# Kernel optimization log

Measured on AMD Instinct MI355X. Metric: run time of the kernel, lower is better.

## Reference

```python
import jax, jax.numpy as jnp
import numpy as np

EMBED_DIM = 768
NUM_HEADS = 12
HEAD_DIM = EMBED_DIM // NUM_HEADS
SCALING = HEAD_DIM ** -0.5
B, N = 4, 2048


def setup_inputs() -> dict:
    key = jax.random.key(0)
    k_x, k_wqkv, k_bqkv, k_wo, k_bo = jax.random.split(key, 5)
    s = EMBED_DIM ** -0.5
    return {
        "x_q": jax.random.normal(k_x, (B, N, EMBED_DIM), dtype=jnp.float32),
        # torch Linear weight layout: (out_features, in_features)
        "w_qkv": jax.random.normal(k_wqkv, (3 * EMBED_DIM, EMBED_DIM), dtype=jnp.float32) * s,
        "b_qkv": jax.random.normal(k_bqkv, (3 * EMBED_DIM,), dtype=jnp.float32) * s,
        "w_out": jax.random.normal(k_wo, (EMBED_DIM, EMBED_DIM), dtype=jnp.float32) * s,
        "b_out": jax.random.normal(k_bo, (EMBED_DIM,), dtype=jnp.float32) * s,
    }


def reference(x_q, w_qkv, b_qkv, w_out, b_out):
    b_sz, n, _ = x_q.shape
    # qkv projection: x @ W^T + b -> (B, N, 3E)
    qkv = jnp.einsum("bne,fe->bnf", x_q, w_qkv) + b_qkv
    # reshape to (B, N, 3, H, D) then move heads: (B, H, 3, N, D)
    qkv = qkv.reshape(b_sz, n, 3, NUM_HEADS, HEAD_DIM).transpose(0, 3, 2, 1, 4)
    q, k, v = qkv[:, :, 0], qkv[:, :, 1], qkv[:, :, 2]
    q = q * SCALING
    # scores (B, H, N, N); att_m == 'Aug' adds constant +1 bias
    attn = jnp.einsum("bhqd,bhkd->bhqk", q, k) + 1.0
    attn = jax.nn.softmax(attn, axis=-1)
    # attn_dropout p=0.0 -> identity
    out = jnp.einsum("bhqk,bhkd->bhqd", attn, v)
    out = out.transpose(0, 2, 1, 3).reshape(b_sz, n, EMBED_DIM)
    return jnp.einsum("bne,fe->bnf", out, w_out) + b_out
```

## Files before the change

kernel.cpp:

```cpp
#include <hip/hip_runtime.h>

typedef unsigned short u16;
typedef unsigned int   u32;
typedef __bf16 bf16x4 __attribute__((ext_vector_type(4)));
typedef __bf16 bf16x8 __attribute__((ext_vector_type(8)));
typedef float  f32x4  __attribute__((ext_vector_type(4)));

__device__ __forceinline__ u16 f2bf(float f) {
  u32 u = __float_as_uint(f);
  u32 r = (u + 0x7fffu + ((u >> 16) & 1u)) >> 16;
  return (u16)r;
}

__device__ __forceinline__ float fexp2(float x) {
  return __builtin_amdgcn_exp2f(x);
}

typedef const __attribute__((address_space(1))) u32* gp1;
typedef __attribute__((address_space(3))) u32* lp3;
__device__ __forceinline__ void gload16(const void* g, void* l) {
  __builtin_amdgcn_global_load_lds((gp1)g, (lp3)l, 16, 0, 0);
}

__device__ __forceinline__ f32x4 mfma16(bf16x8 a, bf16x8 b, f32x4 c) {
  return __builtin_amdgcn_mfma_f32_16x16x32_bf16(a, b, c, 0, 0, 0);
}

__device__ __forceinline__ int swz8(int r) { return (r ^ (r >> 3)) & 7; }

__global__ __launch_bounds__(256) void cast_all(const float* __restrict__ x,
                                                const float* __restrict__ wqkv,
                                                const float* __restrict__ wo,
                                                uint4* __restrict__ dst) {
  int i = blockIdx.x * 256 + threadIdx.x;
  if (i >= 1081344) return;
  const float* s;
  int j;
  if (i < 786432)       { s = x;    j = i; }
  else if (i < 1007616) { s = wqkv; j = i - 786432; }
  else                  { s = wo;   j = i - 1007616; }
  const float4* s4 = (const float4*)s;
  float4 a = s4[2 * j], b = s4[2 * j + 1];
  uint4 o;
  o.x = (u32)f2bf(a.x) | ((u32)f2bf(a.y) << 16);
  o.y = (u32)f2bf(a.z) | ((u32)f2bf(a.w) << 16);
  o.z = (u32)f2bf(b.x) | ((u32)f2bf(b.y) << 16);
  o.w = (u32)f2bf(b.z) | ((u32)f2bf(b.w) << 16);
  dst[i] = o;
}

__global__ __launch_bounds__(256) void gemm_qkv(
    const u16* __restrict__ A, const u16* __restrict__ Bm,
    const float* __restrict__ bias,
    u16* __restrict__ Q, u16* __restrict__ K, u16* __restrict__ V) {
  __shared__ u16 As[128 * 64];
  __shared__ u16 Bs[128 * 64];
  const int tid = threadIdx.x, w = tid >> 6, l = tid & 63;
  const int lr = l & 15, lg = l >> 4;
  const int n0 = blockIdx.x * 128, m0 = blockIdx.y * 128;
  const int wr = (w >> 1) * 64, wc = (w & 1) * 64;
  f32x4 acc[4][4] = {};
  for (int kt = 0; kt < 768; kt += 64) {
    __syncthreads();
    const u16* Ab = A + m0 * 768 + kt;
    const u16* Bb = Bm + n0 * 768 + kt;
#pragma unroll
    for (int i = 0; i < 4; ++i) {
      int c = i * 256 + tid;
      int r = c >> 3, q = c & 7;
      int qs = (q ^ swz8(r)) << 3;
      gload16(Ab + r * 768 + qs, (char*)As + c * 16);
      gload16(Bb + r * 768 + qs, (char*)Bs + c * 16);
    }
    __syncthreads();
    bf16x8 af[4][2], bfr[4][2];
#pragma unroll
    for (int m = 0; m < 4; ++m) {
      int row = wr + m * 16 + lr;
      int sw = swz8(row);
#pragma unroll
      for (int ks = 0; ks < 2; ++ks)
        af[m][ks] = *(const bf16x8*)((char*)As + row * 128 +
                                     (((ks * 4 + lg) ^ sw) << 4));
    }
#pragma unroll
    for (int n = 0; n < 4; ++n) {
      int row = wc + n * 16 + lr;
      int sw = swz8(row);
#pragma unroll
      for (int ks = 0; ks < 2; ++ks)
        bfr[n][ks] = *(const bf16x8*)((char*)Bs + row * 128 +
                                      (((ks * 4 + lg) ^ sw) << 4));
    }
#pragma unroll
    for (int ks = 0; ks < 2; ++ks)
#pragma unroll
      for (int m = 0; m < 4; ++m)
#pragma unroll
        for (int n = 0; n < 4; ++n)
          acc[m][n] = mfma16(af[m][ks], bfr[n][ks], acc[m][n]);
  }
#pragma unroll
  for (int n = 0; n < 4; ++n) {
    int f = n0 + wc + n * 16 + lr;
    float bv = bias[f];
    int three = f / 768;
    int hd = f - three * 768;
    int h = hd >> 6, dd = hd & 63;
    if (three == 2) {
#pragma unroll
      for (int m = 0; m < 4; ++m) {
        int row0 = m0 + wr + m * 16 + lg * 4;
        int b2 = row0 >> 11, ns = row0 & 2047;
        ushort4 pk;
        pk.x = f2bf(acc[m][n][0] + bv);
        pk.y = f2bf(acc[m][n][1] + bv);
        pk.z = f2bf(acc[m][n][2] + bv);
        pk.w = f2bf(acc[m][n][3] + bv);
        *(ushort4*)&V[((size_t)(b2 * 12 + h) * 64 + dd) * 2048 + ns] = pk;
      }
    } else {
      u16* dst = (three == 0) ? Q : K;
      float sc = (three == 0) ? 0.125f * 1.44269504f : 1.0f;
#pragma unroll
      for (int m = 0; m < 4; ++m) {
        int row0 = m0 + wr + m * 16 + lg * 4;
#pragma unroll
        for (int j = 0; j < 4; ++j) {
          int row = row0 + j;
          int b2 = row >> 11, ns = row & 2047;
          float val = (acc[m][n][j] + bv) * sc;
          dst[(((b2 * 12 + h) * 2048 + ns) << 6) + dd] = f2bf(val);
        }
      }
    }
  }
}

__global__ __launch_bounds__(256, 4) void attn_kernel(
    const u16* __restrict__ Q, const u16* __restrict__ K,
    const u16* __restrict__ Vt, u16* __restrict__ O) {
  __shared__ u16 Ks[2][64 * 64];
  __shared__ u16 Vs[2][64 * 64];
  const int tid = threadIdx.x, w = tid >> 6, l = tid & 63;
  const int lr = l & 15, lg = l >> 4;
  int d0i = blockIdx.x;
  int bi = (d0i & 7) * 96 + (d0i >> 3);
  int qt = bi & 15, h = (bi >> 4) % 12, b = bi / 192;
  const u16* Qp = Q + ((size_t)(b * 12 + h) * 2048 + qt * 128) * 64;
  const u16* Kp = K + (size_t)(b * 12 + h) * 2048 * 64;
  const u16* Vp = Vt + (size_t)(b * 12 + h) * 64 * 2048;
  u16* Op = O + (size_t)(b * 2048 + qt * 128) * 768 + h * 64;

  bf16x8 aq[2][2];
#pragma unroll
  for (int mt = 0; mt < 2; ++mt)
#pragma unroll
    for (int ks = 0; ks < 2; ++ks)
      aq[mt][ks] = *(const bf16x8*)&Qp[(w * 32 + mt * 16 + lr) * 64 + ks * 32 + lg * 8];

  bf16x8 vone;
#pragma unroll
  for (int i = 0; i < 8; ++i) vone[i] = (__bf16)1.0f;

  f32x4 aO[2][4] = {};
  f32x4 sacc[2] = {};

#define STAGE(buf, kt)                                                         \
  do {                                                                         \
    const u16* Kt = Kp + (kt) * 4096;                                          \
    const u16* Vg = Vp + (kt) * 64;                                            \
    _Pragma("unroll") for (int i = 0; i < 2; ++i) {                            \
      int c = i * 256 + tid;                                                   \
      int r = c >> 3, q = c & 7;                                               \
      int qs = (q ^ swz8(r)) << 3;                                             \
      gload16(Kt + r * 64 + qs, (char*)Ks[buf] + c * 16);                      \
      gload16(Vg + r * 2048 + qs, (char*)Vs[buf] + c * 16);                    \
    }                                                                          \
  } while (0)

  STAGE(0, 0);
  __syncthreads();

#pragma unroll 2
  for (int kt = 0; kt < 32; ++kt) {
    const int p = kt & 1;
    if (kt < 31) STAGE(p ^ 1, kt + 1);

    f32x4 S[2][4] = {};
    __builtin_amdgcn_s_setprio(1);
#pragma unroll
    for (int nt = 0; nt < 4; ++nt) {
      int row = nt * 16 + lr;
      int sw = swz8(row);
#pragma unroll
      for (int ks = 0; ks < 2; ++ks) {
        bf16x8 a = *(const bf16x8*)((char*)Ks[p] + row * 128 +
                                    (((ks * 4 + lg) ^ sw) << 4));
        S[0][nt] = mfma16(a, aq[0][ks], S[0][nt]);
        S[1][nt] = mfma16(a, aq[1][ks], S[1][nt]);
      }
    }
    __builtin_amdgcn_s_setprio(0);

    bf16x8 ap[2][2];
#pragma unroll
    for (int mt = 0; mt < 2; ++mt) {
      f32x4 pe[4];
#pragma unroll
      for (int nt = 0; nt < 4; ++nt)
#pragma unroll
        for (int j = 0; j < 4; ++j) pe[nt][j] = fexp2(S[mt][nt][j]);
#pragma unroll
      for (int ks = 0; ks < 2; ++ks) {
        bf16x8 f;
#pragma unroll
        for (int j = 0; j < 4; ++j) {
          f[j]     = (__bf16)pe[2 * ks][j];
          f[4 + j] = (__bf16)pe[2 * ks + 1][j];
        }
        ap[mt][ks] = f;
      }
    }

    __builtin_amdgcn_s_setprio(1);
#pragma unroll
    for (int ks = 0; ks < 2; ++ks) {
      sacc[0] = mfma16(ap[0][ks], vone, sacc[0]);
      sacc[1] = mfma16(ap[1][ks], vone, sacc[1]);
#pragma unroll
      for (int dt = 0; dt < 4; ++dt) {
        int row = dt * 16 + lr;
        int sw = swz8(row);
        char* vrow = (char*)Vs[p] + row * 128 + (lg & 1) * 8;
        bf16x4 lo = *(const bf16x4*)(vrow + (((ks * 4 + (lg >> 1)) ^ sw) << 4));
        bf16x4 hi = *(const bf16x4*)(vrow + (((ks * 4 + 2 + (lg >> 1)) ^ sw) << 4));
        bf16x8 bv = __builtin_shufflevector(lo, hi, 0, 1, 2, 3, 4, 5, 6, 7);
        aO[0][dt] = mfma16(ap[0][ks], bv, aO[0][dt]);
        aO[1][dt] = mfma16(ap[1][ks], bv, aO[1][dt]);
      }
    }
    __builtin_amdgcn_s_setprio(0);

    __syncthreads();
  }

#pragma unroll
  for (int mt = 0; mt < 2; ++mt) {
    f32x4 rinv;
#pragma unroll
    for (int j = 0; j < 4; ++j) rinv[j] = 1.0f / sacc[mt][j];
#pragma unroll
    for (int dt = 0; dt < 4; ++dt)
#pragma unroll
      for (int j = 0; j < 4; ++j) {
        int row = w * 32 + mt * 16 + lg * 4 + j;
        Op[(size_t)row * 768 + dt * 16 + lr] = f2bf(aO[mt][dt][j] * rinv[j]);
      }
  }
}

__global__ __launch_bounds__(256) void gemm_out(
    const u16* __restrict__ A, const u16* __restrict__ Bm,
    const float* __restrict__ bias, float* __restrict__ C) {
  __shared__ u16 As[128 * 64];
  __shared__ u16 Bs[128 * 64];
  const int tid = threadIdx.x, w = tid >> 6, l = tid & 63;
  const int lr = l & 15, lg = l >> 4;
  const int n0 = blockIdx.x * 128, m0 = blockIdx.y * 128;
  const int wr = (w >> 1) * 64, wc = (w & 1) * 64;
  f32x4 acc[4][4] = {};
  for (int kt = 0; kt < 768; kt += 64) {
    __syncthreads();
    const u16* Ab = A + m0 * 768 + kt;
    const u16* Bb = Bm + n0 * 768 + kt;
#pragma unroll
    for (int i = 0; i < 4; ++i) {
      int c = i * 256 + tid;
      int r = c >> 3, q = c & 7;
      int qs = (q ^ swz8(r)) << 3;
      gload16(Ab + r * 768 + qs, (char*)As + c * 16);
      gload16(Bb + r * 768 + qs, (char*)Bs + c * 16);
    }
    __syncthreads();
    bf16x8 af[4][2], bfr[4][2];
#pragma unroll
    for (int m = 0; m < 4; ++m) {
      int row = wr + m * 16 + lr;
      int sw = swz8(row);
#pragma unroll
      for (int ks = 0; ks < 2; ++ks)
        af[m][ks] = *(const bf16x8*)((char*)As + row * 128 +
                                     (((ks * 4 + lg) ^ sw) << 4));
    }
#pragma unroll
    for (int n = 0; n < 4; ++n) {
      int row = wc + n * 16 + lr;
      int sw = swz8(row);
#pragma unroll
      for (int ks = 0; ks < 2; ++ks)
        bfr[n][ks] = *(const bf16x8*)((char*)Bs + row * 128 +
                                      (((ks * 4 + lg) ^ sw) << 4));
    }
#pragma unroll
    for (int ks = 0; ks < 2; ++ks)
#pragma unroll
      for (int m = 0; m < 4; ++m)
#pragma unroll
        for (int n = 0; n < 4; ++n)
          acc[m][n] = mfma16(af[m][ks], bfr[n][ks], acc[m][n]);
  }
#pragma unroll
  for (int n = 0; n < 4; ++n) {
    int f = n0 + wc + n * 16 + lr;
    float bv = bias[f];
#pragma unroll
    for (int m = 0; m < 4; ++m) {
      int row0 = m0 + wr + m * 16 + lg * 4;
#pragma unroll
      for (int j = 0; j < 4; ++j) {
        int row = row0 + j;
        C[(size_t)row * 768 + f] = acc[m][n][j] + bv;
      }
    }
  }
}

extern "C" void kernel_launch(void* const* d_in, const int* in_sizes, int n_in,
                              void* d_out, int out_size, void* d_ws, size_t ws_size,
                              hipStream_t stream) {
  const float* x     = (const float*)d_in[0];
  const float* w_qkv = (const float*)d_in[1];
  const float* b_qkv = (const float*)d_in[2];
  const float* w_out = (const float*)d_in[3];
  const float* b_out = (const float*)d_in[4];

  char* ws = (char*)d_ws;
  u16* xb    = (u16*)(ws + 0);
  u16* wqkvb = (u16*)(ws + 12582912);
  u16* wob   = (u16*)(ws + 16121856);
  u16* qb    = (u16*)(ws + 17301504);
  u16* kb    = (u16*)(ws + 29884416);
  u16* vb    = (u16*)(ws + 42467328);
  u16* ob    = (u16*)(ws + 55050240);

  cast_all<<<4224, 256, 0, stream>>>(x, w_qkv, w_out, (uint4*)ws);

  gemm_qkv<<<dim3(18, 64), 256, 0, stream>>>(xb, wqkvb, b_qkv, qb, kb, vb);
  attn_kernel<<<768, 256, 0, stream>>>(qb, kb, vb, ob);
  gemm_out<<<dim3(6, 64), 256, 0, stream>>>(ob, wob, b_out, (float*)d_out);
}
```

Before: 160.7 us.

## Double-buffer GEMM LDS tiles, remap blocks across XCDs, raise MFMA priority

Both projection GEMMs now use two LDS buffers, so the global-to-LDS load of the next K tile is issued while MFMAs run on the current one. The per-iteration sync count drops from two to one. Blocks are launched on a 1D grid and remapped so consecutive ids spread across the 8 XCDs while neighbouring tiles share cache. s_setprio is raised around the MFMA block. LDS use per block doubles to 64KB, which may lower occupancy.

```diff
diff --git a/kernel.cpp b/kernel.cpp
--- a/kernel.cpp
+++ b/kernel.cpp
@@ -53,26 +53,35 @@
     const u16* __restrict__ A, const u16* __restrict__ Bm,
     const float* __restrict__ bias,
     u16* __restrict__ Q, u16* __restrict__ K, u16* __restrict__ V) {
-  __shared__ u16 As[128 * 64];
-  __shared__ u16 Bs[128 * 64];
+  __shared__ u16 As[2][128 * 64];
+  __shared__ u16 Bs[2][128 * 64];
   const int tid = threadIdx.x, w = tid >> 6, l = tid & 63;
   const int lr = l & 15, lg = l >> 4;
-  const int n0 = blockIdx.x * 128, m0 = blockIdx.y * 128;
+  int id = blockIdx.x;
+  int bi = (id & 7) * 144 + (id >> 3);
+  const int m0 = (bi / 18) * 128, n0 = (bi % 18) * 128;
   const int wr = (w >> 1) * 64, wc = (w & 1) * 64;
   f32x4 acc[4][4] = {};
-  for (int kt = 0; kt < 768; kt += 64) {
-    __syncthreads();
-    const u16* Ab = A + m0 * 768 + kt;
-    const u16* Bb = Bm + n0 * 768 + kt;
-#pragma unroll
-    for (int i = 0; i < 4; ++i) {
-      int c = i * 256 + tid;
-      int r = c >> 3, q = c & 7;
-      int qs = (q ^ swz8(r)) << 3;
-      gload16(Ab + r * 768 + qs, (char*)As + c * 16);
-      gload16(Bb + r * 768 + qs, (char*)Bs + c * 16);
-    }
-    __syncthreads();
+
+#define GSTAGE(buf, kt)                                                        \
+  do {                                                                         \
+    const u16* Ab = A + m0 * 768 + (kt);                                       \
+    const u16* Bb = Bm + n0 * 768 + (kt);                                      \
+    _Pragma("unroll") for (int i = 0; i < 4; ++i) {                            \
+      int c = i * 256 + tid;                                                   \
+      int r = c >> 3, q = c & 7;                                               \
+      int qs = (q ^ swz8(r)) << 3;                                             \
+      gload16(Ab + r * 768 + qs, (char*)As[buf] + c * 16);                     \
+      gload16(Bb + r * 768 + qs, (char*)Bs[buf] + c * 16);                     \
+    }                                                                          \
+  } while (0)
+
+  GSTAGE(0, 0);
+  __syncthreads();
+
+  for (int t = 0; t < 12; ++t) {
+    const int buf = t & 1;
+    if (t < 11) GSTAGE(buf ^ 1, (t + 1) * 64);
     bf16x8 af[4][2], bfr[4][2];
 #pragma unroll
     for (int m = 0; m < 4; ++m) {
@@ -80,7 +89,7 @@
       int sw = swz8(row);
 #pragma unroll
       for (int ks = 0; ks < 2; ++ks)
-        af[m][ks] = *(const bf16x8*)((char*)As + row * 128 +
+        af[m][ks] = *(const bf16x8*)((char*)As[buf] + row * 128 +
                                      (((ks * 4 + lg) ^ sw) << 4));
     }
 #pragma unroll
@@ -89,9 +98,10 @@
       int sw = swz8(row);
 #pragma unroll
       for (int ks = 0; ks < 2; ++ks)
-        bfr[n][ks] = *(const bf16x8*)((char*)Bs + row * 128 +
+        bfr[n][ks] = *(const bf16x8*)((char*)Bs[buf] + row * 128 +
                                       (((ks * 4 + lg) ^ sw) << 4));
     }
+    __builtin_amdgcn_s_setprio(1);
 #pragma unroll
     for (int ks = 0; ks < 2; ++ks)
 #pragma unroll
@@ -99,7 +109,10 @@
 #pragma unroll
         for (int n = 0; n < 4; ++n)
           acc[m][n] = mfma16(af[m][ks], bfr[n][ks], acc[m][n]);
-  }
+    __builtin_amdgcn_s_setprio(0);
+    __syncthreads();
+  }
+
 #pragma unroll
   for (int n = 0; n < 4; ++n) {
     int f = n0 + wc + n * 16 + lr;
@@ -263,26 +276,22 @@
 __global__ __launch_bounds__(256) void gemm_out(
     const u16* __restrict__ A, const u16* __restrict__ Bm,
     const float* __restrict__ bias, float* __restrict__ C) {
-  __shared__ u16 As[128 * 64];
-  __shared__ u16 Bs[128 * 64];
+  __shared__ u16 As[2][128 * 64];
+  __shared__ u16 Bs[2][128 * 64];
   const int tid = threadIdx.x, w = tid >> 6, l = tid & 63;
   const int lr = l & 15, lg = l >> 4;
-  const int n0 = blockIdx.x * 128, m0 = blockIdx.y * 128;
+  int id = blockIdx.x;
+  int bi = (id & 7) * 48 + (id >> 3);
+  const int m0 = (bi / 6) * 128, n0 = (bi % 6) * 128;
   const int wr = (w >> 1) * 64, wc = (w & 1) * 64;
   f32x4 acc[4][4] = {};
-  for (int kt = 0; kt < 768; kt += 64) {
-    __syncthreads();
-    const u16* Ab = A + m0 * 768 + kt;
-    const u16* Bb = Bm + n0 * 768 + kt;
-#pragma unroll
-    for (int i = 0; i < 4; ++i) {
-      int c = i * 256 + tid;
-      int r = c >> 3, q = c & 7;
-      int qs = (q ^ swz8(r)) << 3;
-      gload16(Ab + r * 768 + qs, (char*)As + c * 16);
-      gload16(Bb + r * 768 + qs, (char*)Bs + c * 16);
-    }
-    __syncthreads();
+
+  GSTAGE(0, 0);
+  __syncthreads();
+
+  for (int t = 0; t < 12; ++t) {
+    const int buf = t & 1;
+    if (t < 11) GSTAGE(buf ^ 1, (t + 1) * 64);
     bf16x8 af[4][2], bfr[4][2];
 #pragma unroll
     for (int m = 0; m < 4; ++m) {
@@ -290,7 +299,7 @@
       int sw = swz8(row);
 #pragma unroll
       for (int ks = 0; ks < 2; ++ks)
-        af[m][ks] = *(const bf16x8*)((char*)As + row * 128 +
+        af[m][ks] = *(const bf16x8*)((char*)As[buf] + row * 128 +
                                      (((ks * 4 + lg) ^ sw) << 4));
     }
 #pragma unroll
@@ -299,9 +308,10 @@
       int sw = swz8(row);
 #pragma unroll
       for (int ks = 0; ks < 2; ++ks)
-        bfr[n][ks] = *(const bf16x8*)((char*)Bs + row * 128 +
+        bfr[n][ks] = *(const bf16x8*)((char*)Bs[buf] + row * 128 +
                                       (((ks * 4 + lg) ^ sw) << 4));
     }
+    __builtin_amdgcn_s_setprio(1);
 #pragma unroll
     for (int ks = 0; ks < 2; ++ks)
 #pragma unroll
@@ -309,7 +319,10 @@
 #pragma unroll
         for (int n = 0; n < 4; ++n)
           acc[m][n] = mfma16(af[m][ks], bfr[n][ks], acc[m][n]);
-  }
+    __builtin_amdgcn_s_setprio(0);
+    __syncthreads();
+  }
+
 #pragma unroll
   for (int n = 0; n < 4; ++n) {
     int f = n0 + wc + n * 16 + lr;
@@ -346,7 +359,7 @@
 
   cast_all<<<4224, 256, 0, stream>>>(x, w_qkv, w_out, (uint4*)ws);
 
-  gemm_qkv<<<dim3(18, 64), 256, 0, stream>>>(xb, wqkvb, b_qkv, qb, kb, vb);
+  gemm_qkv<<<1152, 256, 0, stream>>>(xb, wqkvb, b_qkv, qb, kb, vb);
   attn_kernel<<<768, 256, 0, stream>>>(qb, kb, vb, ob);
-  gemm_out<<<dim3(6, 64), 256, 0, stream>>>(ob, wob, b_out, (float*)d_out);
-}
+  gemm_out<<<384, 256, 0, stream>>>(ob, wob, b_out, (float*)d_out);
+}
```

Result: faster. 145.4 us (-9.6%).
